# Performance work log

Measured on AMD Instinct MI355X. Metric: run time of the kernel, lower is better.

## Reference

```python
import jax, jax.numpy as jnp
import numpy as np

T = 4.0  # distillation temperature (init kwarg)
B, C = 64, 1000


def _hierarchical_softmax(x, targets):
    # x, targets: [B, C]
    xd = jax.lax.stop_gradient(x)
    # t2[b,i,k] = relu(x[b,i] - stop_grad(x[b,k]))  -> [B, C, C]
    t2 = jnp.maximum(x[:, :, None] - xd[:, None, :], 0.0)
    # t3[b,i] = mean_k targets[b,k] * t2[b,i,k]
    t3 = (targets[:, None, :] * t2).mean(axis=-1)  # [B, C]
    choice = targets * jnp.exp(-t3) + (1.0 - targets)
    ex = jnp.exp(x)
    neg_sum = ((1.0 - targets) * ex).sum(axis=-1, keepdims=True)  # [B, 1]
    return ex / (choice * neg_sum + ex)


def setup_inputs() -> dict:
    key = jax.random.key(0)
    k1, k2, k3 = jax.random.split(key, 3)
    y_s = jax.random.normal(k1, (B, C), dtype=jnp.float32)
    y_t = jax.random.normal(k2, (B, C), dtype=jnp.float32)
    w = jax.random.randint(k3, (B, C), 0, 2).astype(jnp.float32)  # multi-hot targets
    return {"y_s": y_s, "y_t": y_t, "w": w}


def reference(y_s, y_t, w):
    # 'w' branch of DistillKL.forward (dead code: preds/thr/sigmoid/max_min omitted)
    p_s = _hierarchical_softmax(y_s / 4.0, w)
    p_t = _hierarchical_softmax(y_t / 4.0, w)
    p_s_1 = jnp.minimum(p_s, 1.0)  # clamp(max=1)
    p_t_1 = jnp.minimum(p_t, 1.0)
    # abs(...) >= 0 so clamp(min=0,max=1) == min(.,1)
    pos_expo = w * jnp.minimum(jnp.abs((p_t_1 + 1.0) / 2.0 - p_s_1), 1.0) ** 0.25
    neg_expo = (1.0 - w) * jnp.minimum(jnp.abs(p_t_1 / 2.0 - p_s_1), 1.0)
    expt = pos_expo + neg_expo
    ps = jnp.maximum(p_s_1 ** expt, 1e-7)
    pt = jnp.maximum(p_t, 1e-7)
    # my_kl: -(target * log(pred)).sum(dim=1).mean() * T**2
    return -(pt * jnp.log(ps)).sum(axis=1).mean() * (T * T)
```

## Files before the change

### kernel.cpp

```cpp
#include <hip/hip_runtime.h>


#define BN 64
#define CN 1000
#define SPLITS 8
#define CHUNK 125
#define THREADS 128
#define NEG_LOG_EPS -16.118095650958319f

__global__ __launch_bounds__(THREADS) void distill_part(
    const float* __restrict__ ys, const float* __restrict__ yt,
    const float* __restrict__ w, float* __restrict__ part)
{
    const int b = blockIdx.x;
    const int s = blockIdx.y;
    const int tid = threadIdx.x;
    const int lane = tid & 63;
    const int wid = tid >> 6;

    __shared__ float xs[CN], xt[CN];
    __shared__ float xsm[CN], xtm[CN];
    __shared__ float wsh[CN];
    __shared__ float redns[4];
    __shared__ float redterm[2];

    const float* ysr = ys + b * CN;
    const float* ytr = yt + b * CN;
    const float* wr  = w  + b * CN;

    float ns_s = 0.f, ns_t = 0.f;
    for (int k = tid; k < CN; k += THREADS) {
        float a  = ysr[k] * 0.25f;
        float c2 = ytr[k] * 0.25f;
        float wk = wr[k];
        xs[k] = a; xt[k] = c2; wsh[k] = wk;
        bool pos = (wk != 0.f);
        xsm[k] = pos ? a  : 1e30f;
        xtm[k] = pos ? c2 : 1e30f;
        float nw = 1.f - wk;
        ns_s += nw * expf(a);
        ns_t += nw * expf(c2);
    }
    #pragma unroll
    for (int off = 32; off > 0; off >>= 1) {
        ns_s += __shfl_down(ns_s, off);
        ns_t += __shfl_down(ns_t, off);
    }
    if (lane == 0) { redns[wid * 2] = ns_s; redns[wid * 2 + 1] = ns_t; }
    __syncthreads();
    const float negsum_s = redns[0] + redns[2];
    const float negsum_t = redns[1] + redns[3];

    float term = 0.f;
    const int i = s * CHUNK + tid;
    if (tid < CHUNK && i < CN) {
        const float xsi = xs[i], xti = xt[i];
        float acc_s = 0.f, acc_t = 0.f;
        #pragma unroll 4
        for (int k = 0; k < CN; ++k) {
            acc_s += fmaxf(xsi - xsm[k], 0.f);
            acc_t += fmaxf(xti - xtm[k], 0.f);
        }
        const float t3s = acc_s * (1.0f / CN);
        const float t3t = acc_t * (1.0f / CN);
        const float wi = wsh[i];
        const float ch_s = wi * expf(-t3s) + (1.f - wi);
        const float ch_t = wi * expf(-t3t) + (1.f - wi);
        const float exs = expf(xsi), ext = expf(xti);
        const float p_s = exs / (ch_s * negsum_s + exs);
        const float p_t = ext / (ch_t * negsum_t + ext);
        const float ps1 = fminf(p_s, 1.f);
        const float pt1 = fminf(p_t, 1.f);
        const float vpos = fminf(fabsf((pt1 + 1.f) * 0.5f - ps1), 1.f);
        const float vneg = fminf(fabsf(pt1 * 0.5f - ps1), 1.f);
        const float expt = wi * sqrtf(sqrtf(vpos)) + (1.f - wi) * vneg;
        const float logps = fmaxf(expt * logf(ps1), NEG_LOG_EPS);
        term = fmaxf(p_t, 1e-7f) * logps;
    }
    #pragma unroll
    for (int off = 32; off > 0; off >>= 1) term += __shfl_down(term, off);
    __syncthreads();
    if (lane == 0) redterm[wid] = term;
    __syncthreads();
    if (tid == 0) part[b * SPLITS + s] = redterm[0] + redterm[1];
}

__global__ __launch_bounds__(64) void distill_final(
    const float* __restrict__ part, float* __restrict__ out)
{
    const int t = threadIdx.x;
    float v = 0.f;
    for (int j = t; j < BN * SPLITS; j += 64) v += part[j];
    #pragma unroll
    for (int off = 32; off > 0; off >>= 1) v += __shfl_down(v, off);
    if (t == 0) out[0] = -0.25f * v;
}

extern "C" void kernel_launch(void* const* d_in, const int* in_sizes, int n_in,
                              void* d_out, int out_size, void* d_ws, size_t ws_size,
                              hipStream_t stream) {
    const float* ys = (const float*)d_in[0];
    const float* yt = (const float*)d_in[1];
    const float* w  = (const float*)d_in[2];
    float* out  = (float*)d_out;
    float* part = (float*)d_ws;

    dim3 grid(BN, SPLITS);
    distill_part<<<grid, THREADS, 0, stream>>>(ys, yt, w, part);
    distill_final<<<1, 64, 0, stream>>>(part, out);
}
```

Baseline: 83.15 us.

## Use min identity, interleaved float2 LDS layout and split accumulators in pairwise loop

Rewrites relu(x_i - m_k) summed over k as x_i minus the sum of min(x_i, m_k), dropping a subtract per inner iteration. Packs the masked student and teacher values into one float2 shared array for wider LDS loads, and splits the reduction into four independent accumulators for instruction-level parallelism. Also switches to fast __expf/__logf intrinsics, reads x_i and w_i straight from global memory, and removes a redundant barrier. The fast intrinsics and reassociated sums slightly change floating-point results.

```diff
diff --git a/kernel.cpp b/kernel.cpp
--- a/kernel.cpp
+++ b/kernel.cpp
@@ -18,9 +18,7 @@
     const int lane = tid & 63;
     const int wid = tid >> 6;
 
-    __shared__ float xs[CN], xt[CN];
-    __shared__ float xsm[CN], xtm[CN];
-    __shared__ float wsh[CN];
+    __shared__ float2 xm[CN];
     __shared__ float redns[4];
     __shared__ float redterm[2];
 
@@ -33,13 +31,11 @@
         float a  = ysr[k] * 0.25f;
         float c2 = ytr[k] * 0.25f;
         float wk = wr[k];
-        xs[k] = a; xt[k] = c2; wsh[k] = wk;
         bool pos = (wk != 0.f);
-        xsm[k] = pos ? a  : 1e30f;
-        xtm[k] = pos ? c2 : 1e30f;
+        xm[k] = make_float2(pos ? a : 1e30f, pos ? c2 : 1e30f);
         float nw = 1.f - wk;
-        ns_s += nw * expf(a);
-        ns_t += nw * expf(c2);
+        ns_s += nw * __expf(a);
+        ns_t += nw * __expf(c2);
     }
     #pragma unroll
     for (int off = 32; off > 0; off >>= 1) {
@@ -54,19 +50,28 @@
     float term = 0.f;
     const int i = s * CHUNK + tid;
     if (tid < CHUNK && i < CN) {
-        const float xsi = xs[i], xti = xt[i];
-        float acc_s = 0.f, acc_t = 0.f;
-        #pragma unroll 4
-        for (int k = 0; k < CN; ++k) {
-            acc_s += fmaxf(xsi - xsm[k], 0.f);
-            acc_t += fmaxf(xti - xtm[k], 0.f);
+        const float xsi = ysr[i] * 0.25f;
+        const float xti = ytr[i] * 0.25f;
+        const float wi  = wr[i];
+        float as0 = 0.f, as1 = 0.f, as2 = 0.f, as3 = 0.f;
+        float at0 = 0.f, at1 = 0.f, at2 = 0.f, at3 = 0.f;
+        for (int k = 0; k < CN; k += 4) {
+            float2 m0 = xm[k + 0];
+            float2 m1 = xm[k + 1];
+            float2 m2 = xm[k + 2];
+            float2 m3 = xm[k + 3];
+            as0 += fminf(xsi, m0.x);  at0 += fminf(xti, m0.y);
+            as1 += fminf(xsi, m1.x);  at1 += fminf(xti, m1.y);
+            as2 += fminf(xsi, m2.x);  at2 += fminf(xti, m2.y);
+            as3 += fminf(xsi, m3.x);  at3 += fminf(xti, m3.y);
         }
-        const float t3s = acc_s * (1.0f / CN);
-        const float t3t = acc_t * (1.0f / CN);
-        const float wi = wsh[i];
-        const float ch_s = wi * expf(-t3s) + (1.f - wi);
-        const float ch_t = wi * expf(-t3t) + (1.f - wi);
-        const float exs = expf(xsi), ext = expf(xti);
+        const float acc_s = (as0 + as1) + (as2 + as3);
+        const float acc_t = (at0 + at1) + (at2 + at3);
+        const float t3s = xsi - acc_s * (1.0f / CN);
+        const float t3t = xti - acc_t * (1.0f / CN);
+        const float ch_s = wi * __expf(-t3s) + (1.f - wi);
+        const float ch_t = wi * __expf(-t3t) + (1.f - wi);
+        const float exs = __expf(xsi), ext = __expf(xti);
         const float p_s = exs / (ch_s * negsum_s + exs);
         const float p_t = ext / (ch_t * negsum_t + ext);
         const float ps1 = fminf(p_s, 1.f);
@@ -74,12 +79,11 @@
         const float vpos = fminf(fabsf((pt1 + 1.f) * 0.5f - ps1), 1.f);
         const float vneg = fminf(fabsf(pt1 * 0.5f - ps1), 1.f);
         const float expt = wi * sqrtf(sqrtf(vpos)) + (1.f - wi) * vneg;
-        const float logps = fmaxf(expt * logf(ps1), NEG_LOG_EPS);
+        const float logps = fmaxf(expt * __logf(ps1), NEG_LOG_EPS);
         term = fmaxf(p_t, 1e-7f) * logps;
     }
     #pragma unroll
     for (int off = 32; off > 0; off >>= 1) term += __shfl_down(term, off);
-    __syncthreads();
     if (lane == 0) redterm[wid] = term;
     __syncthreads();
     if (tid == 0) part[b * SPLITS + s] = redterm[0] + redterm[1];
```

Result: no change. 84.19 us (+1.3%).
